# Performance work log

Hardware: AMD Instinct MI355X
Metric: run time of the kernel (lower is better)

The kernel has to match this reference:

```python
import jax, jax.numpy as jnp
import numpy as np

EPS = 1e-5


def setup_inputs() -> dict:
    key = jax.random.key(0)
    k1, k2, k3, k4, k5 = jax.random.split(key, 5)
    N, d, F = 8192, 768, 32768
    return {
        "x": jax.random.normal(k1, (N, d), dtype=jnp.float32),
        "pre_bias": jax.random.normal(k2, (d,), dtype=jnp.float32) * 0.02,
        "latent_bias": jax.random.normal(k3, (F,), dtype=jnp.float32) * 0.02,
        "enc_w": jax.random.normal(k4, (F, d), dtype=jnp.float32) / np.sqrt(d),
        "dec_w": jax.random.normal(k5, (d, F), dtype=jnp.float32) / np.sqrt(F),
        "k": 32,
    }


def reference(x, pre_bias, latent_bias, enc_w, dec_w, k):
    # --- encode: manual layernorm (keep mean/std for de-norm) ---
    mean = jnp.mean(x, axis=-1, keepdims=True)           # (N,1)
    var = jnp.var(x, axis=-1, keepdims=True)             # unbiased=False
    std = jnp.sqrt(var + EPS)
    x_centered = (x - mean) / std - pre_bias             # (N,d)
    h_pre = x_centered @ enc_w.T + latent_bias           # (N,F)
    # --- top-k ReLU: keep k largest pre-activations, relu them ---
    topk_vals, topk_idx = jax.lax.top_k(h_pre, k)        # (N,k)
    h = jnp.put_along_axis(jnp.zeros_like(h_pre), topk_idx,
                           jax.nn.relu(topk_vals), axis=-1, inplace=False)
    # --- decode + de-normalize ---
    x_rec_norm = h @ dec_w.T + pre_bias                  # (N,d)
    x_hat = x_rec_norm * std + mean
    return x_hat
```

## Files before the change

kernel.cpp:

```cpp
#include <hip/hip_runtime.h>
#include <hip/hip_bf16.h>
#include <stdint.h>

#define N_ROWS 8192
#define DIM 768
#define NF 32768
#define TOPK 32
#define CANDCAP 72
#define RTHRESH 44

typedef __attribute__((ext_vector_type(8))) short bf16x8;
typedef __attribute__((ext_vector_type(8))) short short8;
typedef __attribute__((ext_vector_type(4))) float f32x4;

__device__ inline void async_ld16(const void* g, void* l) {
  __builtin_amdgcn_global_load_lds(
      (const __attribute__((address_space(1))) unsigned int*)g,
      (__attribute__((address_space(3))) unsigned int*)l, 16, 0, 0);
}

__device__ inline unsigned short f2bf(float f) {
  union { float f; unsigned u; } c; c.f = f;
  unsigned r = c.u + 0x7FFFu + ((c.u >> 16) & 1u);
  return (unsigned short)(r >> 16);
}

__device__ inline float bf2f(unsigned short u) {
  union { unsigned u; float f; } c; c.u = ((unsigned)u) << 16;
  return c.f;
}

__device__ inline void block_barrier_fenced() {
  __builtin_amdgcn_s_barrier();
  asm volatile("" ::: "memory");
  __builtin_amdgcn_sched_barrier(0);
}

__global__ __launch_bounds__(256) void k_ln(const float* __restrict__ x,
                                            const float* __restrict__ pre_bias,
                                            unsigned short* __restrict__ xh,
                                            float* __restrict__ meanA,
                                            float* __restrict__ stdA) {
  int row = blockIdx.x;
  int tid = threadIdx.x;
  int lane = tid & 63, wv = tid >> 6;
  const float* xr = x + (size_t)row * DIM;
  float a0 = xr[tid], a1 = xr[tid + 256], a2 = xr[tid + 512];
  __shared__ float red[8];
  float s = a0 + a1 + a2;
  for (int off = 32; off > 0; off >>= 1) s += __shfl_down(s, off);
  if (lane == 0) red[wv] = s;
  __syncthreads();
  float mean;
  if (tid == 0) { mean = (red[0] + red[1] + red[2] + red[3]) / (float)DIM; red[4] = mean; }
  __syncthreads();
  mean = red[4];
  float d0 = a0 - mean, d1 = a1 - mean, d2 = a2 - mean;
  float ss = d0 * d0 + d1 * d1 + d2 * d2;
  for (int off = 32; off > 0; off >>= 1) ss += __shfl_down(ss, off);
  if (lane == 0) red[wv] = ss;
  __syncthreads();
  float stdv;
  if (tid == 0) {
    float var = (red[0] + red[1] + red[2] + red[3]) / (float)DIM;
    stdv = sqrtf(var + 1e-5f);
    red[5] = stdv;
    meanA[row] = mean;
    stdA[row] = stdv;
  }
  __syncthreads();
  stdv = red[5];
  float inv = 1.0f / stdv;
  unsigned short* xo = xh + (size_t)row * DIM;
  xo[tid]       = f2bf(d0 * inv - pre_bias[tid]);
  xo[tid + 256] = f2bf(d1 * inv - pre_bias[tid + 256]);
  xo[tid + 512] = f2bf(d2 * inv - pre_bias[tid + 512]);
}

__global__ __launch_bounds__(256) void k_cv(const float* __restrict__ w,
                                            unsigned short* __restrict__ o, int n4) {
  int i = blockIdx.x * 256 + threadIdx.x;
  if (i >= n4) return;
  float4 v = ((const float4*)w)[i];
  ushort4 r;
  r.x = f2bf(v.x); r.y = f2bf(v.y); r.z = f2bf(v.z); r.w = f2bf(v.w);
  ((ushort4*)o)[i] = r;
}

__global__ __launch_bounds__(256) void k_tr(const float* __restrict__ dec,
                                            unsigned short* __restrict__ dect) {
  __shared__ float t[32][33];
  int tx = threadIdx.x & 31, ty = threadIdx.x >> 5;
  int fb = blockIdx.x * 32, cb = blockIdx.y * 32;
  for (int i = 0; i < 4; i++) {
    int r = ty + i * 8;
    t[r][tx] = dec[(size_t)(cb + r) * NF + fb + tx];
  }
  __syncthreads();
  for (int i = 0; i < 4; i++) {
    int r = ty + i * 8;
    dect[(size_t)(fb + r) * DIM + cb + tx] = f2bf(t[tx][r]);
  }
}

__global__ __launch_bounds__(512, 4) void k_gemm(const unsigned short* __restrict__ xh,
                                                 const unsigned short* __restrict__ ench,
                                                 const float* __restrict__ latent_bias,
                                                 unsigned* __restrict__ cand6) {
  __shared__ __align__(16) char smem[78336];
  int tid = threadIdx.x;
  int lane = tid & 63;
  int w = tid >> 6;
  int wr = w >> 2, wc = w & 3;
  int lid = blockIdx.x + blockIdx.y * gridDim.x;
  int xcd = lid & 7;
  int sprime = lid >> 9;
  int u = (lid >> 3) & 63;
  int bx = sprime * 8 + (u & 7);
  int by = xcd * 8 + (u >> 3);
  const int fr = lane & 15, hi = lane >> 4;

  const char* Ab = (const char*)(xh + (size_t)by * 128 * DIM);
  const char* Bb = (const char*)(ench + (size_t)bx * 128 * DIM);

  int rA[2], cA[2];
#pragma unroll
  for (int i = 0; i < 2; i++) {
    int L = i * 8192 + tid * 16;
    int r = L >> 7;
    rA[i] = r;
    cA[i] = (L & 127) ^ ((r & 7) << 4);
  }

  f32x4 acc[4][2];
#pragma unroll
  for (int m = 0; m < 4; m++)
#pragma unroll
    for (int n = 0; n < 2; n++) {
      f32x4 z = {0.f, 0.f, 0.f, 0.f};
      acc[m][n] = z;
    }

#define STAGE(kt, b)                                                          \
  do {                                                                        \
    char* dA = smem + (b) * 16384;                                            \
    char* dB = smem + 32768 + (b) * 16384;                                    \
    _Pragma("unroll") for (int i = 0; i < 2; i++)                             \
        async_ld16(Ab + (size_t)rA[i] * (DIM * 2) + (kt) * 128 + cA[i],       \
                   dA + i * 8192 + tid * 16);                                 \
    _Pragma("unroll") for (int i = 0; i < 2; i++)                             \
        async_ld16(Bb + (size_t)rA[i] * (DIM * 2) + (kt) * 128 + cA[i],       \
                   dB + i * 8192 + tid * 16);                                 \
  } while (0)

  STAGE(0, 0);

  for (int kt = 0; kt < 12; kt++) {
    int b = kt & 1;
    if (kt + 1 < 12) {
      STAGE(kt + 1, (kt + 1) & 1);
      asm volatile("s_waitcnt vmcnt(4)" ::: "memory");
    } else {
      asm volatile("s_waitcnt vmcnt(0)" ::: "memory");
    }
    block_barrier_fenced();

    const char* pA = smem + b * 16384;
    const char* pB = smem + 32768 + b * 16384;
#pragma unroll
    for (int kh = 0; kh < 2; kh++) {
      int cbb = kh * 64 + hi * 16;
      bf16x8 af[4], bv[2];
#pragma unroll
      for (int m = 0; m < 4; m++) {
        int row = wr * 64 + m * 16 + fr;
        af[m] = *(const bf16x8*)(pA + row * 128 + (cbb ^ ((row & 7) << 4)));
      }
#pragma unroll
      for (int n = 0; n < 2; n++) {
        int row = wc * 32 + n * 16 + fr;
        bv[n] = *(const bf16x8*)(pB + row * 128 + (cbb ^ ((row & 7) << 4)));
      }
      __builtin_amdgcn_s_setprio(1);
#pragma unroll
      for (int m = 0; m < 4; m++)
#pragma unroll
        for (int n = 0; n < 2; n++)
          acc[m][n] = __builtin_amdgcn_mfma_f32_16x16x32_bf16(af[m], bv[n], acc[m][n], 0, 0, 0);
      __builtin_amdgcn_s_setprio(0);
    }
    block_barrier_fenced();
  }
#undef STAGE

  float* sC = (float*)smem;
  int* m6 = (int*)(smem + 66048);
#pragma unroll
  for (int n = 0; n < 2; n++) {
    int lcol = wc * 32 + n * 16 + fr;
    float lbv = latent_bias[bx * 128 + lcol];
#pragma unroll
    for (int m = 0; m < 4; m++) {
      int lrow = wr * 64 + m * 16 + hi * 4;
#pragma unroll
      for (int j = 0; j < 4; j++)
        sC[(lrow + j) * 129 + lcol] = acc[m][n][j] + lbv;
    }
  }
  __syncthreads();
  {
    int r = tid & 127, q = tid >> 7;
    const float* cr = sC + r * 129 + q * 32;
    unsigned c0 = 0, c1 = 0, c2 = 0, c3 = 0, c4 = 0, c5 = 0;
    for (int c = 0; c < 32; c++) {
      union { float f; unsigned u; } cv; cv.f = cr[c];
      unsigned key = ((int)cv.u < 0) ? ~cv.u : (cv.u | 0x80000000u);
      unsigned pk = (key & 0xFFFFFF00u) | (unsigned)(q * 32 + c);
      if (pk > c0) {
        bool b1 = pk > c1, b2 = pk > c2, b3 = pk > c3, b4 = pk > c4, b5 = pk > c5;
        c0 = b1 ? c1 : pk;
        c1 = b1 ? (b2 ? c2 : pk) : c1;
        c2 = b2 ? (b3 ? c3 : pk) : c2;
        c3 = b3 ? (b4 ? c4 : pk) : c3;
        c4 = b4 ? (b5 ? c5 : pk) : c4;
        c5 = b5 ? pk : c5;
      }
    }
    int* mp = m6 + (r * 4 + q) * 6;
    mp[0] = (int)c0; mp[1] = (int)c1; mp[2] = (int)c2;
    mp[3] = (int)c3; mp[4] = (int)c4; mp[5] = (int)c5;
  }
  __syncthreads();
  if (tid < 128) {
    const int* L0 = m6 + (tid * 4 + 0) * 6;
    const int* L1 = m6 + (tid * 4 + 1) * 6;
    const int* L2 = m6 + (tid * 4 + 2) * 6;
    const int* L3 = m6 + (tid * 4 + 3) * 6;
    int i0 = 5, i1 = 5, i2 = 5, i3 = 5;
    unsigned* dst = cand6 + ((size_t)(by * 128 + tid) * 256 + bx) * 6;
#pragma unroll
    for (int k = 0; k < 6; k++) {
      unsigned v0 = (i0 >= 0) ? (unsigned)L0[i0] : 0u;
      unsigned v1 = (i1 >= 0) ? (unsigned)L1[i1] : 0u;
      unsigned v2 = (i2 >= 0) ? (unsigned)L2[i2] : 0u;
      unsigned v3 = (i3 >= 0) ? (unsigned)L3[i3] : 0u;
      unsigned best = v0; int bq = 0;
      if (v1 > best) { best = v1; bq = 1; }
      if (v2 > best) { best = v2; bq = 2; }
      if (v3 > best) { best = v3; bq = 3; }
      dst[k] = best;
      if (bq == 0) i0--; else if (bq == 1) i1--; else if (bq == 2) i2--; else i3--;
    }
  }
}

__global__ __launch_bounds__(256) void k_screen(const unsigned* __restrict__ cand6,
                                                int* __restrict__ cntg,
                                                int* __restrict__ candg) {
  __shared__ int hist[512];
  __shared__ int hist2[128];
  __shared__ int sb_bstar, sb_chi, sb_cnt;
  __shared__ unsigned sb_tau;
  __shared__ int cand[CANDCAP];

  int tid = threadIdx.x, lane = tid & 63;
  int row = blockIdx.x;
  const unsigned* src = cand6 + (size_t)row * 1536 + tid * 6;
  unsigned pc0 = src[0], pc1 = src[1], pc2 = src[2],
           pc3 = src[3], pc4 = src[4], pc5 = src[5];

  hist[tid] = 0; hist[tid + 256] = 0;
  if (tid < 128) hist2[tid] = 0;
  if (tid == 0) sb_cnt = 0;
  __syncthreads();

  atomicAdd(&hist[pc0 >> 23], 1);
  atomicAdd(&hist[pc1 >> 23], 1);
  atomicAdd(&hist[pc2 >> 23], 1);
  atomicAdd(&hist[pc3 >> 23], 1);
  atomicAdd(&hist[pc4 >> 23], 1);
  atomicAdd(&hist[pc5 >> 23], 1);
  __syncthreads();

  if (tid < 64) {
    int b = lane * 8;
    int h0 = hist[b], h1 = hist[b+1], h2 = hist[b+2], h3 = hist[b+3];
    int h4 = hist[b+4], h5 = hist[b+5], h6 = hist[b+6], h7 = hist[b+7];
    int s7 = h7, s6 = h6 + s7, s5 = h5 + s6, s4 = h4 + s5;
    int s3 = h3 + s4, s2 = h2 + s3, s1 = h1 + s2, s0 = h0 + s1;
    int tot = s0, acc = tot;
#pragma unroll
    for (int off = 1; off <= 32; off <<= 1) {
      int t = __shfl_down(acc, off);
      if (lane + off < 64) acc += t;
    }
    int excl = acc - tot;
    int best = -1, bs = 0, hb = 0;
    if (excl + s0 >= RTHRESH) { best = b + 0; bs = excl + s0; hb = h0; }
    if (excl + s1 >= RTHRESH) { best = b + 1; bs = excl + s1; hb = h1; }
    if (excl + s2 >= RTHRESH) { best = b + 2; bs = excl + s2; hb = h2; }
    if (excl + s3 >= RTHRESH) { best = b + 3; bs = excl + s3; hb = h3; }
    if (excl + s4 >= RTHRESH) { best = b + 4; bs = excl + s4; hb = h4; }
    if (excl + s5 >= RTHRESH) { best = b + 5; bs = excl + s5; hb = h5; }
    if (excl + s6 >= RTHRESH) { best = b + 6; bs = excl + s6; hb = h6; }
    if (excl + s7 >= RTHRESH) { best = b + 7; bs = excl + s7; hb = h7; }
#pragma unroll
    for (int off = 32; off > 0; off >>= 1) {
      int ob = __shfl_down(best, off), obs = __shfl_down(bs, off), ohb = __shfl_down(hb, off);
      if (lane + off < 64 && ob > best) { best = ob; bs = obs; hb = ohb; }
    }
    if (lane == 0) { sb_bstar = best; sb_chi = bs - hb; }
  }
  __syncthreads();
  int bstar = sb_bstar, chi = sb_chi;

  if ((int)(pc0 >> 23) == bstar) atomicAdd(&hist2[(pc0 >> 16) & 127], 1);
  if ((int)(pc1 >> 23) == bstar) atomicAdd(&hist2[(pc1 >> 16) & 127], 1);
  if ((int)(pc2 >> 23) == bstar) atomicAdd(&hist2[(pc2 >> 16) & 127], 1);
  if ((int)(pc3 >> 23) == bstar) atomicAdd(&hist2[(pc3 >> 16) & 127], 1);
  if ((int)(pc4 >> 23) == bstar) atomicAdd(&hist2[(pc4 >> 16) & 127], 1);
  if ((int)(pc5 >> 23) == bstar) atomicAdd(&hist2[(pc5 >> 16) & 127], 1);
  __syncthreads();

  if (tid < 64) {
    int g0 = hist2[lane * 2], g1 = hist2[lane * 2 + 1];
    int s1 = g1, s0 = g0 + g1;
    int tot = s0, acc = tot;
#pragma unroll
    for (int off = 1; off <= 32; off <<= 1) {
      int t = __shfl_down(acc, off);
      if (lane + off < 64) acc += t;
    }
    int excl = acc - tot;
    int best = -1;
    if (chi + excl + s0 >= RTHRESH) best = lane * 2;
    if (chi + excl + s1 >= RTHRESH) best = lane * 2 + 1;
#pragma unroll
    for (int off = 32; off > 0; off >>= 1) {
      int ob = __shfl_down(best, off);
      if (lane + off < 64 && ob > best) best = ob;
    }
    if (lane == 0) sb_tau = ((unsigned)((bstar << 7) | best)) << 16;
  }
  __syncthreads();

  unsigned tau = sb_tau;
#define EMIT(PC)                                                   \
  if ((PC) >= tau) {                                               \
    int pos = atomicAdd(&sb_cnt, 1);                               \
    if (pos < CANDCAP) cand[pos] = tid * 128 + (int)((PC) & 127u); \
  }
  EMIT(pc0) EMIT(pc1) EMIT(pc2) EMIT(pc3) EMIT(pc4) EMIT(pc5)
#undef EMIT
  __syncthreads();

  int cnt = sb_cnt < CANDCAP ? sb_cnt : CANDCAP;
  if (tid == 0) cntg[row] = cnt;
  if (tid < CANDCAP) candg[(size_t)row * CANDCAP + tid] = (tid < cnt) ? cand[tid] : 0;
}

__global__ __launch_bounds__(256) void k_sel(const float* __restrict__ x,
                                             const float* __restrict__ pre_bias,
                                             const float* __restrict__ latent_bias,
                                             const float* __restrict__ enc,
                                             const unsigned short* __restrict__ dect,
                                             const int* __restrict__ cntg,
                                             const int* __restrict__ candg,
                                             const float* __restrict__ meanA,
                                             const float* __restrict__ stdA,
                                             float* __restrict__ out) {
  __shared__ __align__(16) float xn[DIM];
  __shared__ float exactv[128];
  __shared__ int self_[128];
  __shared__ float hv[TOPK];
  __shared__ int hf[TOPK];

  int row = blockIdx.x, tid = threadIdx.x, lane = tid & 63;
  float m = meanA[row], s = stdA[row], inv = 1.0f / s;
  const float* xr = x + (size_t)row * DIM;
  for (int i = tid; i < DIM; i += 256)
    xn[i] = (xr[i] - m) * inv - pre_bias[i];
  int cnt = cntg[row];
  if (tid < 128) {
    self_[tid] = (tid < cnt) ? candg[(size_t)row * CANDCAP + tid] : 0x7FFFFFF;
    exactv[tid] = -3.0e38f;
  }
  __syncthreads();

#pragma unroll
  for (int pass = 0; pass < 2; pass++) {
    int g = pass * 64 + (tid >> 2), t4 = tid & 3;
    if (g < cnt) {
      int f = self_[g];
      const float4* xp = (const float4*)xn;
      const float4* wp = (const float4*)(enc + (size_t)f * DIM);
      float acc = 0.f;
#pragma unroll 4
      for (int i = t4; i < DIM / 4; i += 4) {
        float4 a = xp[i], b = wp[i];
        acc = fmaf(a.x, b.x, acc);
        acc = fmaf(a.y, b.y, acc);
        acc = fmaf(a.z, b.z, acc);
        acc = fmaf(a.w, b.w, acc);
      }
      acc += __shfl_xor(acc, 1);
      acc += __shfl_xor(acc, 2);
      if (t4 == 0) exactv[g] = acc + latent_bias[f];
    }
  }
  __syncthreads();

  if (tid < 64) {
    float v0 = exactv[lane];      int f0 = self_[lane];
    float v1 = exactv[lane + 64]; int f1 = self_[lane + 64];
    for (int r = 0; r < TOPK; r++) {
      float bv = v0; int bf = f0;
      if (v1 > bv || (v1 == bv && f1 < bf)) { bv = v1; bf = f1; }
#pragma unroll
      for (int off = 32; off > 0; off >>= 1) {
        float ov = __shfl_down(bv, off);
        int of = __shfl_down(bf, off);
        if (lane + off < 64 && (ov > bv || (ov == bv && of < bf))) { bv = ov; bf = of; }
      }
      bv = __shfl(bv, 0);
      bf = __shfl(bf, 0);
      if (lane == 0) { hv[r] = bv > 0.f ? bv : 0.f; hf[r] = bf; }
      if (f0 == bf) v0 = -3.0e38f;
      if (f1 == bf) v1 = -3.0e38f;
    }
  }
  __syncthreads();

  float* orow = out + (size_t)row * DIM;
#pragma unroll
  for (int t = 0; t < 3; t++) {
    int c = tid + t * 256;
    float acc = pre_bias[c];
    for (int j = 0; j < TOPK; j++)
      acc = fmaf(hv[j], bf2f(dect[(size_t)hf[j] * DIM + c]), acc);
    orow[c] = acc * s + m;
  }
}

extern "C" void kernel_launch(void* const* d_in, const int* in_sizes, int n_in,
                              void* d_out, int out_size, void* d_ws, size_t ws_size,
                              hipStream_t stream) {
  const float* x   = (const float*)d_in[0];
  const float* pb  = (const float*)d_in[1];
  const float* lb  = (const float*)d_in[2];
  const float* enc = (const float*)d_in[3];
  const float* dec = (const float*)d_in[4];
  float* out = (float*)d_out;

  const size_t off_xh   = 0;
  const size_t off_ench = 12582912;
  const size_t off_dect = 62914560;
  const size_t off_mean = 113246208;
  const size_t off_std  = 113278976;
  const size_t off_cnt  = 113311744;
  const size_t off_cand = 113344512;
  const size_t off_c6   = 115703808;
  if (ws_size < 166035456) return;

  char* ws = (char*)d_ws;
  unsigned short* xh   = (unsigned short*)(ws + off_xh);
  unsigned short* ench = (unsigned short*)(ws + off_ench);
  unsigned short* dect = (unsigned short*)(ws + off_dect);
  float* meanA = (float*)(ws + off_mean);
  float* stdA  = (float*)(ws + off_std);
  int*   cntg  = (int*)(ws + off_cnt);
  int*   candg = (int*)(ws + off_cand);
  unsigned* cand6 = (unsigned*)(ws + off_c6);

  hipLaunchKernelGGL(k_ln, dim3(N_ROWS), dim3(256), 0, stream, x, pb, xh, meanA, stdA);
  hipLaunchKernelGGL(k_cv, dim3((NF * DIM / 4 + 255) / 256), dim3(256), 0, stream,
                     enc, ench, NF * DIM / 4);
  hipLaunchKernelGGL(k_tr, dim3(NF / 32, DIM / 32), dim3(256), 0, stream, dec, dect);

  hipLaunchKernelGGL(k_gemm, dim3(NF / 128, N_ROWS / 128), dim3(512), 0, stream,
                     xh, ench, lb, cand6);
  hipLaunchKernelGGL(k_screen, dim3(N_ROWS), dim3(256), 0, stream, cand6, cntg, candg);

  hipLaunchKernelGGL(k_sel, dim3(N_ROWS), dim3(256), 0, stream,
                     x, pb, lb, enc, dect, cntg, candg, meanA, stdA, out);
}
```

Measured before the change: 862.6 us.

## Enlarge encoder GEMM tile to 256x128 with 4x4 MFMA per wave

New measurement: 854.9 us. Within noise of the previous version (-0.9%).

```diff
diff --git a/kernel.cpp b/kernel.cpp
--- a/kernel.cpp
+++ b/kernel.cpp
@@ -111,32 +111,56 @@
   int tid = threadIdx.x;
   int lane = tid & 63;
   int w = tid >> 6;
-  int wr = w >> 2, wc = w & 3;
+  int wr = w >> 1, wc = w & 1;
   int lid = blockIdx.x + blockIdx.y * gridDim.x;
   int xcd = lid & 7;
-  int sprime = lid >> 9;
-  int u = (lid >> 3) & 63;
-  int bx = sprime * 8 + (u & 7);
-  int by = xcd * 8 + (u >> 3);
+  int u = (lid >> 3) & 31;
+  int s = lid >> 8;
+  int bx = s * 8 + (u & 7);
+  int by = xcd * 4 + (u >> 3);
   const int fr = lane & 15, hi = lane >> 4;
 
-  const char* Ab = (const char*)(xh + (size_t)by * 128 * DIM);
+  const char* Ab = (const char*)(xh + (size_t)by * 256 * DIM);
   const char* Bb = (const char*)(ench + (size_t)bx * 128 * DIM);
 
-  int rA[2], cA[2];
+  int rA[2], cA[2], rB, cB;
 #pragma unroll
   for (int i = 0; i < 2; i++) {
     int L = i * 8192 + tid * 16;
-    int r = L >> 7;
-    rA[i] = r;
-    cA[i] = (L & 127) ^ ((r & 7) << 4);
-  }
-
-  f32x4 acc[4][2];
+    int R = L >> 7;
+    int ss = ((L >> 4) & 7) ^ (R & 7);
+    rA[i] = (R << 1) + (ss >> 2);
+    cA[i] = (ss & 3) << 4;
+  }
+  {
+    int L = tid * 16;
+    int R = L >> 7;
+    int ss = ((L >> 4) & 7) ^ (R & 7);
+    rB = (R << 1) + (ss >> 2);
+    cB = (ss & 3) << 4;
+  }
+
+  int offA[4], offB[4];
+#pragma unroll
+  for (int m = 0; m < 4; m++) {
+    int r = wr * 64 + m * 16 + fr;
+    int R = r >> 1;
+    int slot = ((r & 1) << 2) + hi;
+    offA[m] = R * 128 + ((slot ^ (R & 7)) << 4);
+  }
+#pragma unroll
+  for (int n = 0; n < 4; n++) {
+    int r = wc * 64 + n * 16 + fr;
+    int R = r >> 1;
+    int slot = ((r & 1) << 2) + hi;
+    offB[n] = R * 128 + ((slot ^ (R & 7)) << 4);
+  }
+
+  f32x4 acc[4][4];
 #pragma unroll
   for (int m = 0; m < 4; m++)
 #pragma unroll
-    for (int n = 0; n < 2; n++) {
+    for (int n = 0; n < 4; n++) {
       f32x4 z = {0.f, 0.f, 0.f, 0.f};
       acc[m][n] = z;
     }
@@ -144,51 +168,40 @@
 #define STAGE(kt, b)                                                          \
   do {                                                                        \
     char* dA = smem + (b) * 16384;                                            \
-    char* dB = smem + 32768 + (b) * 16384;                                    \
+    char* dB = smem + 32768 + (b) * 8192;                                     \
     _Pragma("unroll") for (int i = 0; i < 2; i++)                             \
-        async_ld16(Ab + (size_t)rA[i] * (DIM * 2) + (kt) * 128 + cA[i],       \
+        async_ld16(Ab + (size_t)rA[i] * (DIM * 2) + (kt) * 64 + cA[i],        \
                    dA + i * 8192 + tid * 16);                                 \
-    _Pragma("unroll") for (int i = 0; i < 2; i++)                             \
-        async_ld16(Bb + (size_t)rA[i] * (DIM * 2) + (kt) * 128 + cA[i],       \
-                   dB + i * 8192 + tid * 16);                                 \
+    async_ld16(Bb + (size_t)rB * (DIM * 2) + (kt) * 64 + cB,                  \
+               dB + tid * 16);                                                \
   } while (0)
 
   STAGE(0, 0);
 
-  for (int kt = 0; kt < 12; kt++) {
+  for (int kt = 0; kt < 24; kt++) {
     int b = kt & 1;
-    if (kt + 1 < 12) {
+    if (kt + 1 < 24) {
       STAGE(kt + 1, (kt + 1) & 1);
-      asm volatile("s_waitcnt vmcnt(4)" ::: "memory");
+      asm volatile("s_waitcnt vmcnt(3)" ::: "memory");
     } else {
       asm volatile("s_waitcnt vmcnt(0)" ::: "memory");
     }
     block_barrier_fenced();
 
     const char* pA = smem + b * 16384;
-    const char* pB = smem + 32768 + b * 16384;
-#pragma unroll
-    for (int kh = 0; kh < 2; kh++) {
-      int cbb = kh * 64 + hi * 16;
-      bf16x8 af[4], bv[2];
-#pragma unroll
-      for (int m = 0; m < 4; m++) {
-        int row = wr * 64 + m * 16 + fr;
-        af[m] = *(const bf16x8*)(pA + row * 128 + (cbb ^ ((row & 7) << 4)));
-      }
-#pragma unroll
-      for (int n = 0; n < 2; n++) {
-        int row = wc * 32 + n * 16 + fr;
-        bv[n] = *(const bf16x8*)(pB + row * 128 + (cbb ^ ((row & 7) << 4)));
-      }
-      __builtin_amdgcn_s_setprio(1);
-#pragma unroll
-      for (int m = 0; m < 4; m++)
-#pragma unroll
-        for (int n = 0; n < 2; n++)
-          acc[m][n] = __builtin_amdgcn_mfma_f32_16x16x32_bf16(af[m], bv[n], acc[m][n], 0, 0, 0);
-      __builtin_amdgcn_s_setprio(0);
-    }
+    const char* pB = smem + 32768 + b * 8192;
+    bf16x8 af[4], bv[4];
+#pragma unroll
+    for (int m = 0; m < 4; m++) af[m] = *(const bf16x8*)(pA + offA[m]);
+#pragma unroll
+    for (int n = 0; n < 4; n++) bv[n] = *(const bf16x8*)(pB + offB[n]);
+    __builtin_amdgcn_s_setprio(1);
+#pragma unroll
+    for (int m = 0; m < 4; m++)
+#pragma unroll
+      for (int n = 0; n < 4; n++)
+        acc[m][n] = __builtin_amdgcn_mfma_f32_16x16x32_bf16(af[m], bv[n], acc[m][n], 0, 0, 0);
+    __builtin_amdgcn_s_setprio(0);
     block_barrier_fenced();
   }
 #undef STAGE
@@ -196,61 +209,67 @@
   float* sC = (float*)smem;
   int* m6 = (int*)(smem + 66048);
 #pragma unroll
-  for (int n = 0; n < 2; n++) {
-    int lcol = wc * 32 + n * 16 + fr;
-    float lbv = latent_bias[bx * 128 + lcol];
-#pragma unroll
-    for (int m = 0; m < 4; m++) {
-      int lrow = wr * 64 + m * 16 + hi * 4;
-#pragma unroll
-      for (int j = 0; j < 4; j++)
-        sC[(lrow + j) * 129 + lcol] = acc[m][n][j] + lbv;
-    }
-  }
-  __syncthreads();
-  {
-    int r = tid & 127, q = tid >> 7;
-    const float* cr = sC + r * 129 + q * 32;
-    unsigned c0 = 0, c1 = 0, c2 = 0, c3 = 0, c4 = 0, c5 = 0;
-    for (int c = 0; c < 32; c++) {
-      union { float f; unsigned u; } cv; cv.f = cr[c];
-      unsigned key = ((int)cv.u < 0) ? ~cv.u : (cv.u | 0x80000000u);
-      unsigned pk = (key & 0xFFFFFF00u) | (unsigned)(q * 32 + c);
-      if (pk > c0) {
-        bool b1 = pk > c1, b2 = pk > c2, b3 = pk > c3, b4 = pk > c4, b5 = pk > c5;
-        c0 = b1 ? c1 : pk;
-        c1 = b1 ? (b2 ? c2 : pk) : c1;
-        c2 = b2 ? (b3 ? c3 : pk) : c2;
-        c3 = b3 ? (b4 ? c4 : pk) : c3;
-        c4 = b4 ? (b5 ? c5 : pk) : c4;
-        c5 = b5 ? pk : c5;
+  for (int p = 0; p < 2; p++) {
+    if ((wr >> 1) == p) {
+#pragma unroll
+      for (int n = 0; n < 4; n++) {
+        int lcol = wc * 64 + n * 16 + fr;
+        float lbv = latent_bias[bx * 128 + lcol];
+#pragma unroll
+        for (int m = 0; m < 4; m++) {
+          int lr = (wr & 1) * 64 + m * 16 + hi * 4;
+#pragma unroll
+          for (int j = 0; j < 4; j++)
+            sC[(lr + j) * 129 + lcol] = acc[m][n][j] + lbv;
+        }
       }
     }
-    int* mp = m6 + (r * 4 + q) * 6;
-    mp[0] = (int)c0; mp[1] = (int)c1; mp[2] = (int)c2;
-    mp[3] = (int)c3; mp[4] = (int)c4; mp[5] = (int)c5;
-  }
-  __syncthreads();
-  if (tid < 128) {
-    const int* L0 = m6 + (tid * 4 + 0) * 6;
-    const int* L1 = m6 + (tid * 4 + 1) * 6;
-    const int* L2 = m6 + (tid * 4 + 2) * 6;
-    const int* L3 = m6 + (tid * 4 + 3) * 6;
-    int i0 = 5, i1 = 5, i2 = 5, i3 = 5;
-    unsigned* dst = cand6 + ((size_t)(by * 128 + tid) * 256 + bx) * 6;
-#pragma unroll
-    for (int k = 0; k < 6; k++) {
-      unsigned v0 = (i0 >= 0) ? (unsigned)L0[i0] : 0u;
-      unsigned v1 = (i1 >= 0) ? (unsigned)L1[i1] : 0u;
-      unsigned v2 = (i2 >= 0) ? (unsigned)L2[i2] : 0u;
-      unsigned v3 = (i3 >= 0) ? (unsigned)L3[i3] : 0u;
-      unsigned best = v0; int bq = 0;
-      if (v1 > best) { best = v1; bq = 1; }
-      if (v2 > best) { best = v2; bq = 2; }
-      if (v3 > best) { best = v3; bq = 3; }
-      dst[k] = best;
-      if (bq == 0) i0--; else if (bq == 1) i1--; else if (bq == 2) i2--; else i3--;
-    }
+    __syncthreads();
+    {
+      int r = tid & 127, q = tid >> 7;
+      const float* cr = sC + r * 129 + q * 32;
+      unsigned c0 = 0, c1 = 0, c2 = 0, c3 = 0, c4 = 0, c5 = 0;
+      for (int c = 0; c < 32; c++) {
+        union { float f; unsigned u; } cv; cv.f = cr[c];
+        unsigned key = ((int)cv.u < 0) ? ~cv.u : (cv.u | 0x80000000u);
+        unsigned pk = (key & 0xFFFFFF00u) | (unsigned)(q * 32 + c);
+        if (pk > c0) {
+          bool b1 = pk > c1, b2 = pk > c2, b3 = pk > c3, b4 = pk > c4, b5 = pk > c5;
+          c0 = b1 ? c1 : pk;
+          c1 = b1 ? (b2 ? c2 : pk) : c1;
+          c2 = b2 ? (b3 ? c3 : pk) : c2;
+          c3 = b3 ? (b4 ? c4 : pk) : c3;
+          c4 = b4 ? (b5 ? c5 : pk) : c4;
+          c5 = b5 ? pk : c5;
+        }
+      }
+      int* mp = m6 + (r * 4 + q) * 6;
+      mp[0] = (int)c0; mp[1] = (int)c1; mp[2] = (int)c2;
+      mp[3] = (int)c3; mp[4] = (int)c4; mp[5] = (int)c5;
+    }
+    __syncthreads();
+    if (tid < 128) {
+      const int* L0 = m6 + (tid * 4 + 0) * 6;
+      const int* L1 = m6 + (tid * 4 + 1) * 6;
+      const int* L2 = m6 + (tid * 4 + 2) * 6;
+      const int* L3 = m6 + (tid * 4 + 3) * 6;
+      int i0 = 5, i1 = 5, i2 = 5, i3 = 5;
+      unsigned* dst = cand6 + ((size_t)(by * 256 + p * 128 + tid) * 256 + bx) * 6;
+#pragma unroll
+      for (int k = 0; k < 6; k++) {
+        unsigned v0 = (i0 >= 0) ? (unsigned)L0[i0] : 0u;
+        unsigned v1 = (i1 >= 0) ? (unsigned)L1[i1] : 0u;
+        unsigned v2 = (i2 >= 0) ? (unsigned)L2[i2] : 0u;
+        unsigned v3 = (i3 >= 0) ? (unsigned)L3[i3] : 0u;
+        unsigned best = v0; int bq = 0;
+        if (v1 > best) { best = v1; bq = 1; }
+        if (v2 > best) { best = v2; bq = 2; }
+        if (v3 > best) { best = v3; bq = 3; }
+        dst[k] = best;
+        if (bq == 0) i0--; else if (bq == 1) i1--; else if (bq == 2) i2--; else i3--;
+      }
+    }
+    __syncthreads();
   }
 }
 
@@ -477,7 +496,7 @@
                      enc, ench, NF * DIM / 4);
   hipLaunchKernelGGL(k_tr, dim3(NF / 32, DIM / 32), dim3(256), 0, stream, dec, dect);
 
-  hipLaunchKernelGGL(k_gemm, dim3(NF / 128, N_ROWS / 128), dim3(512), 0, stream,
+  hipLaunchKernelGGL(k_gemm, dim3(NF / 128, N_ROWS / 256), dim3(512), 0, stream,
                      xh, ench, lb, cand6);
   hipLaunchKernelGGL(k_screen, dim3(N_ROWS), dim3(256), 0, stream, cand6, cntg, candg);
 
```
